# Optimization experiments

Hardware: AMD Instinct MI355X
Metric: run time of the kernel (lower is better)

The kernel has to match this reference:

```python
import jax, jax.numpy as jnp
import numpy as np

B, T, I, H, G = 4096, 1024, 1, 16, 48  # G = 3*H gates

def _gru_layer(inp, w_ih, w_hh, b_ih, b_hh):
    # inp: [B, T, Din] -> out: [B, T, H]. PyTorch GRU gate math.
    # Precompute all input-side gate projections once (batched GEMM).
    xg = jnp.einsum('btd,gd->tbg', inp, w_ih) + b_ih  # [T, B, 3H]

    def step(h, xg_t):
        hg = h @ w_hh.T + b_hh                         # [B, 3H]
        xr, xz, xn = jnp.split(xg_t, 3, axis=-1)
        hr, hz, hn = jnp.split(hg, 3, axis=-1)
        r = jax.nn.sigmoid(xr + hr)
        z = jax.nn.sigmoid(xz + hz)
        n = jnp.tanh(xn + r * hn)
        h_new = (1.0 - z) * n + z * h
        return h_new, h_new

    h0 = jnp.zeros((inp.shape[0], H), dtype=inp.dtype)
    _, ys = jax.lax.scan(step, h0, xg)                 # ys: [T, B, H]
    return jnp.transpose(ys, (1, 0, 2))                # [B, T, H]

def setup_inputs() -> dict:
    key = jax.random.key(0)
    ks = jax.random.split(key, 8)
    s = 1.0 / np.sqrt(H)  # PyTorch default uniform(-1/sqrt(H), 1/sqrt(H))
    u = lambda k, shape: jax.random.uniform(k, shape, jnp.float32, -s, s)
    return {
        'x':      jax.random.normal(ks[0], (B, T, I), jnp.float32),
        'w_ih0':  u(ks[1], (G, I)),
        'w_ih12': u(ks[2], (2, G, H)),
        'w_hh':   u(ks[3], (3, G, H)),
        'b_ih':   u(ks[4], (3, G)),
        'b_hh':   u(ks[5], (3, G)),
        'fc_w':   u(ks[6], (5, H)),
        'fc_b':   u(ks[7], (5,)),
    }

def reference(x, w_ih0, w_ih12, w_hh, b_ih, b_hh, fc_w, fc_b):
    # 3-layer GRU (dropout=0.3 between layers is identity in eval mode)
    h = _gru_layer(x, w_ih0,     w_hh[0], b_ih[0], b_hh[0])
    h = _gru_layer(h, w_ih12[0], w_hh[1], b_ih[1], b_hh[1])
    h = _gru_layer(h, w_ih12[1], w_hh[2], b_ih[2], b_hh[2])
    # Linear head on the last timestep
    return h[:, -1, :] @ fc_w.T + fc_b                 # [B, 5]
```

## Files before the change

kernel.cpp:

```cpp
#include <hip/hip_runtime.h>
#include <stdint.h>

#define TSTEPS 1024
#define S 4
#define NK 258
#define L2E 1.4426950408889634f
#define XPITCH 1028

typedef float v2f __attribute__((ext_vector_type(2)));
typedef float v4f __attribute__((ext_vector_type(4)));

__device__ __forceinline__ float rcpf_(float v) { return __builtin_amdgcn_rcpf(v); }
__device__ __forceinline__ float ex2(float v) { return __builtin_amdgcn_exp2f(v); }
#define PKFMA(a, b, c) __builtin_elementwise_fma((a), (b), (c))

__device__ __forceinline__ v2f ldg2(const float* p) {
    v2f r; uint64_t a = (uint64_t)p;
    asm volatile("global_load_dwordx2 %0, %1, off\n\ts_waitcnt vmcnt(0)"
                 : "=v"(r) : "v"(a));
    return r;
}
__device__ __forceinline__ float ldg1(const float* p) {
    float r; uint64_t a = (uint64_t)p;
    asm volatile("global_load_dword %0, %1, off\n\ts_waitcnt vmcnt(0)"
                 : "=v"(r) : "v"(a));
    return r;
}

#define RDH(dst, p)                                                        \
    do {                                                                   \
        v4f a0 = *(const v4f*)(p);                                         \
        v4f a1 = *(const v4f*)((p) + 4);                                   \
        v4f a2 = *(const v4f*)((p) + 8);                                   \
        v4f a3 = *(const v4f*)((p) + 12);                                  \
        dst[0] = __builtin_shufflevector(a0, a0, 0, 1);                    \
        dst[1] = __builtin_shufflevector(a0, a0, 2, 3);                    \
        dst[2] = __builtin_shufflevector(a1, a1, 0, 1);                    \
        dst[3] = __builtin_shufflevector(a1, a1, 2, 3);                    \
        dst[4] = __builtin_shufflevector(a2, a2, 0, 1);                    \
        dst[5] = __builtin_shufflevector(a2, a2, 2, 3);                    \
        dst[6] = __builtin_shufflevector(a3, a3, 0, 1);                    \
        dst[7] = __builtin_shufflevector(a3, a3, 2, 3);                    \
    } while (0)

#define DOT8(w, h, seed)                                                   \
    ({                                                                     \
        v2f _a = PKFMA(w[0], h[0], (seed));                                \
        _a = PKFMA(w[1], h[1], _a); _a = PKFMA(w[2], h[2], _a);            \
        _a = PKFMA(w[3], h[3], _a); _a = PKFMA(w[4], h[4], _a);            \
        _a = PKFMA(w[5], h[5], _a); _a = PKFMA(w[6], h[6], _a);            \
        _a = PKFMA(w[7], h[7], _a);                                        \
        _a.x + _a.y;                                                       \
    })
#define DOT16(wa, ha, wb, hb, seed)                                        \
    ({                                                                     \
        v2f _a = PKFMA(wa[0], ha[0], (seed));                              \
        _a = PKFMA(wa[1], ha[1], _a); _a = PKFMA(wa[2], ha[2], _a);        \
        _a = PKFMA(wa[3], ha[3], _a); _a = PKFMA(wa[4], ha[4], _a);        \
        _a = PKFMA(wa[5], ha[5], _a); _a = PKFMA(wa[6], ha[6], _a);        \
        _a = PKFMA(wa[7], ha[7], _a);                                      \
        _a = PKFMA(wb[0], hb[0], _a); _a = PKFMA(wb[1], hb[1], _a);        \
        _a = PKFMA(wb[2], hb[2], _a); _a = PKFMA(wb[3], hb[3], _a);        \
        _a = PKFMA(wb[4], hb[4], _a); _a = PKFMA(wb[5], hb[5], _a);        \
        _a = PKFMA(wb[6], hb[6], _a); _a = PKFMA(wb[7], hb[7], _a);        \
        _a.x + _a.y;                                                       \
    })

__global__ __launch_bounds__(192, 3)
__attribute__((amdgpu_waves_per_eu(3, 3)))
void gru3_sk(
    const float* __restrict__ x,
    const float* __restrict__ w_ih0,
    const float* __restrict__ w_ih12,
    const float* __restrict__ w_hh,
    const float* __restrict__ b_ih,
    const float* __restrict__ b_hh,
    const float* __restrict__ fc_w,
    const float* __restrict__ fc_b,
    float* __restrict__ out)
{
    __shared__ float xs[4][XPITCH];
    __shared__ float hring[3][2][S][4][16];
    __shared__ float h2f[4][16];

    const int tid = threadIdx.x;
    const int role = tid >> 6;
    const int lane = tid & 63;
    const int s = lane >> 4;
    const int u = lane & 15;
    const int seq = blockIdx.x * 4 + s;

    {
        const float4* xg = (const float4*)(x + (size_t)blockIdx.x * 4 * TSTEPS);
#pragma unroll
        for (int j = 0; j < 6; ++j) {
            int idx = tid + 192 * j;
            if (idx < 1024) {
                float4 v = xg[idx];
                *(float4*)&xs[idx >> 8][(idx & 255) * 4] = v;
            }
        }
#pragma unroll
        for (int j = 0; j < 8; ++j)
            ((float*)hring)[tid + 192 * j] = 0.f;
    }
    __syncthreads();

    if (role == 0) {
        v2f wr[8], wz[8], wn[8];
#pragma unroll
        for (int m = 0; m < 8; ++m) {
            wr[m] = ldg2(w_hh + (u) * 16 + 2 * m) * -L2E;
            wz[m] = ldg2(w_hh + (16 + u) * 16 + 2 * m) * -L2E;
            wn[m] = ldg2(w_hh + (32 + u) * 16 + 2 * m) * (2.f * L2E);
        }
        const float wxr = ldg1(w_ih0 + u) * -L2E;
        const float wxz = ldg1(w_ih0 + 16 + u) * -L2E;
        const float wxn = ldg1(w_ih0 + 32 + u) * (2.f * L2E);
        const v2f sbr = {-(ldg1(b_ih + u) + ldg1(b_hh + u)) * L2E, 0.f};
        const v2f sbz = {-(ldg1(b_ih + 16 + u) + ldg1(b_hh + 16 + u)) * L2E, 0.f};
        const v2f sbn = {ldg1(b_hh + 32 + u) * (2.f * L2E), 0.f};
        const float bnx = ldg1(b_ih + 32 + u) * (2.f * L2E);
        float* cur = &hring[0][0][0][s][0];
        float* prv = &hring[0][1][0][s][0];
        float hown = 0.f;
        for (int K = 0; K < NK; ++K) {
            if (K < 256) {
                v4f xq = *(const v4f*)&xs[s][K * S];
#pragma unroll
                for (int j = 0; j < S; ++j) {
                    const float* rb = (j == 0) ? (prv + (S - 1) * 64)
                                               : (cur + (j - 1) * 64);
                    v2f hp[8];
                    RDH(hp, rb);
                    float xt = xq[j];
                    float sr = fmaf(wxr, xt, DOT8(wr, hp, sbr));
                    float sz = fmaf(wxz, xt, DOT8(wz, hp, sbz));
                    float snh = DOT8(wn, hp, sbn);
                    float r = rcpf_(1.f + ex2(sr));
                    float z = rcpf_(1.f + ex2(sz));
                    float ut = fmaf(r, snh, fmaf(wxn, xt, bnx));
                    float n = fmaf(-2.f, rcpf_(ex2(ut) + 1.f), 1.f);
                    hown = fmaf(z, hown - n, n);
                    cur[j * 64 + u] = hown;
                }
            }
            __syncthreads();
            float* t_ = cur; cur = prv; prv = t_;
        }
    } else if (role == 1) {
        v2f wr[8], wz[8], wn[8], vr[8], vz[8], vn[8];
#pragma unroll
        for (int m = 0; m < 8; ++m) {
            wr[m] = ldg2(w_hh + (48 + u) * 16 + 2 * m) * -L2E;
            wz[m] = ldg2(w_hh + (48 + 16 + u) * 16 + 2 * m) * -L2E;
            wn[m] = ldg2(w_hh + (48 + 32 + u) * 16 + 2 * m) * (2.f * L2E);
            vr[m] = ldg2(w_ih12 + (u) * 16 + 2 * m) * -L2E;
            vz[m] = ldg2(w_ih12 + (16 + u) * 16 + 2 * m) * -L2E;
            vn[m] = ldg2(w_ih12 + (32 + u) * 16 + 2 * m) * (2.f * L2E);
        }
        const v2f sbr = {-(ldg1(b_ih + 48 + u) + ldg1(b_hh + 48 + u)) * L2E, 0.f};
        const v2f sbz = {-(ldg1(b_ih + 64 + u) + ldg1(b_hh + 64 + u)) * L2E, 0.f};
        const v2f sbn = {ldg1(b_hh + 80 + u) * (2.f * L2E), 0.f};
        const v2f sbx = {ldg1(b_ih + 80 + u) * (2.f * L2E), 0.f};
        float* in0 = &hring[0][0][0][s][0];
        float* in1 = &hring[0][1][0][s][0];
        float* my0 = &hring[1][0][0][s][0];
        float* my1 = &hring[1][1][0][s][0];
        float* inp = in1;
        float* mycur = my0; float* myprv = my1;
        float hown = 0.f;
        for (int K = 0; K < NK; ++K) {
            if (K >= 1 && K < 257) {
#pragma unroll
                for (int j = 0; j < S; ++j) {
                    const float* rin = inp + j * 64;
                    const float* rown = (j == 0) ? (myprv + (S - 1) * 64)
                                                 : (mycur + (j - 1) * 64);
                    v2f hin[8], hp[8];
                    RDH(hin, rin);
                    RDH(hp, rown);
                    float sr = DOT16(wr, hp, vr, hin, sbr);
                    float sz = DOT16(wz, hp, vz, hin, sbz);
                    float snh = DOT8(wn, hp, sbn);
                    float snx = DOT8(vn, hin, sbx);
                    float r = rcpf_(1.f + ex2(sr));
                    float z = rcpf_(1.f + ex2(sz));
                    float ut = fmaf(r, snh, snx);
                    float n = fmaf(-2.f, rcpf_(ex2(ut) + 1.f), 1.f);
                    hown = fmaf(z, hown - n, n);
                    mycur[j * 64 + u] = hown;
                }
            }
            __syncthreads();
            float* t_ = inp == in0 ? in1 : in0; inp = t_;
            t_ = mycur; mycur = myprv; myprv = t_;
        }
    } else {
        v2f wr[8], wz[8], wn[8], vr[8], vz[8], vn[8];
#pragma unroll
        for (int m = 0; m < 8; ++m) {
            wr[m] = ldg2(w_hh + (96 + u) * 16 + 2 * m) * -L2E;
            wz[m] = ldg2(w_hh + (96 + 16 + u) * 16 + 2 * m) * -L2E;
            wn[m] = ldg2(w_hh + (96 + 32 + u) * 16 + 2 * m) * (2.f * L2E);
            vr[m] = ldg2(w_ih12 + (48 + u) * 16 + 2 * m) * -L2E;
            vz[m] = ldg2(w_ih12 + (48 + 16 + u) * 16 + 2 * m) * -L2E;
            vn[m] = ldg2(w_ih12 + (48 + 32 + u) * 16 + 2 * m) * (2.f * L2E);
        }
        const v2f sbr = {-(ldg1(b_ih + 96 + u) + ldg1(b_hh + 96 + u)) * L2E, 0.f};
        const v2f sbz = {-(ldg1(b_ih + 112 + u) + ldg1(b_hh + 112 + u)) * L2E, 0.f};
        const v2f sbn = {ldg1(b_hh + 128 + u) * (2.f * L2E), 0.f};
        const v2f sbx = {ldg1(b_ih + 128 + u) * (2.f * L2E), 0.f};
        float* in0 = &hring[1][0][0][s][0];
        float* in1 = &hring[1][1][0][s][0];
        float* my0 = &hring[2][0][0][s][0];
        float* my1 = &hring[2][1][0][s][0];
        float* inp = in1;
        float* mycur = my0; float* myprv = my1;
        float hown = 0.f;
        for (int K = 0; K < NK; ++K) {
            if (K >= 2) {
#pragma unroll
                for (int j = 0; j < S; ++j) {
                    const float* rin = inp + j * 64;
                    const float* rown = (j == 0) ? (myprv + (S - 1) * 64)
                                                 : (mycur + (j - 1) * 64);
                    v2f hin[8], hp[8];
                    RDH(hin, rin);
                    RDH(hp, rown);
                    float sr = DOT16(wr, hp, vr, hin, sbr);
                    float sz = DOT16(wz, hp, vz, hin, sbz);
                    float snh = DOT8(wn, hp, sbn);
                    float snx = DOT8(vn, hin, sbx);
                    float r = rcpf_(1.f + ex2(sr));
                    float z = rcpf_(1.f + ex2(sz));
                    float ut = fmaf(r, snh, snx);
                    float n = fmaf(-2.f, rcpf_(ex2(ut) + 1.f), 1.f);
                    hown = fmaf(z, hown - n, n);
                    mycur[j * 64 + u] = hown;
                }
            }
            __syncthreads();
            float* t_ = inp == in0 ? in1 : in0; inp = t_;
            t_ = mycur; mycur = myprv; myprv = t_;
        }
        h2f[s][u] = hown;
        if (u < 5) {
            float acc = fc_b[u];
#pragma unroll
            for (int j = 0; j < 16; ++j)
                acc = fmaf(fc_w[u * 16 + j], h2f[s][j], acc);
            out[seq * 5 + u] = acc;
        }
    }
}

extern "C" void kernel_launch(void* const* d_in, const int* in_sizes, int n_in,
                              void* d_out, int out_size, void* d_ws, size_t ws_size,
                              hipStream_t stream) {
    const float* x      = (const float*)d_in[0];
    const float* w_ih0  = (const float*)d_in[1];
    const float* w_ih12 = (const float*)d_in[2];
    const float* w_hh   = (const float*)d_in[3];
    const float* b_ih   = (const float*)d_in[4];
    const float* b_hh   = (const float*)d_in[5];
    const float* fc_w   = (const float*)d_in[6];
    const float* fc_b   = (const float*)d_in[7];
    float* out = (float*)d_out;

    gru3_sk<<<1024, 192, 0, stream>>>(
        x, w_ih0, w_ih12, w_hh, b_ih, b_hh, fc_w, fc_b, out);
}
```

Measured before the change: 492.3 us.

## Have each layer compute the next layer's input projections and drop the x LDS staging

Each producer wave now computes the next layer's input-side gate projections (W_ih·h plus bias) right after updating its hidden state and writes them to a shared ring. The consumer layer only reads three scalars per step instead of a 16-wide vector, which shortens its recurrence-critical dot products from 32-length to 16-length. The hidden state is kept in a tiny per-layer scratch in LDS, and x is streamed directly from global memory with a one-step prefetch instead of being staged in LDS. This balances work across the three pipeline waves and cuts LDS use, but it relies on wave-level ordering of the LDS write and the immediate read-back of h within a single wave, and it adds global-load latency for x.

```diff
diff --git a/kernel.cpp b/kernel.cpp
--- a/kernel.cpp
+++ b/kernel.cpp
@@ -5,7 +5,6 @@
 #define S 4
 #define NK 258
 #define L2E 1.4426950408889634f
-#define XPITCH 1028
 
 typedef float v2f __attribute__((ext_vector_type(2)));
 typedef float v4f __attribute__((ext_vector_type(4)));
@@ -52,23 +51,10 @@
         _a = PKFMA(w[7], h[7], _a);                                        \
         _a.x + _a.y;                                                       \
     })
-#define DOT16(wa, ha, wb, hb, seed)                                        \
-    ({                                                                     \
-        v2f _a = PKFMA(wa[0], ha[0], (seed));                              \
-        _a = PKFMA(wa[1], ha[1], _a); _a = PKFMA(wa[2], ha[2], _a);        \
-        _a = PKFMA(wa[3], ha[3], _a); _a = PKFMA(wa[4], ha[4], _a);        \
-        _a = PKFMA(wa[5], ha[5], _a); _a = PKFMA(wa[6], ha[6], _a);        \
-        _a = PKFMA(wa[7], ha[7], _a);                                      \
-        _a = PKFMA(wb[0], hb[0], _a); _a = PKFMA(wb[1], hb[1], _a);        \
-        _a = PKFMA(wb[2], hb[2], _a); _a = PKFMA(wb[3], hb[3], _a);        \
-        _a = PKFMA(wb[4], hb[4], _a); _a = PKFMA(wb[5], hb[5], _a);        \
-        _a = PKFMA(wb[6], hb[6], _a); _a = PKFMA(wb[7], hb[7], _a);        \
-        _a.x + _a.y;                                                       \
-    })
 
 __global__ __launch_bounds__(192, 3)
 __attribute__((amdgpu_waves_per_eu(3, 3)))
-void gru3_sk(
+void gru3_po(
     const float* __restrict__ x,
     const float* __restrict__ w_ih0,
     const float* __restrict__ w_ih12,
@@ -79,9 +65,8 @@
     const float* __restrict__ fc_b,
     float* __restrict__ out)
 {
-    __shared__ float xs[4][XPITCH];
-    __shared__ float hring[3][2][S][4][16];
-    __shared__ float h2f[4][16];
+    __shared__ float pring[2][2][S][4][48];
+    __shared__ float hscr[3][4][16];
 
     const int tid = threadIdx.x;
     const int role = tid >> 6;
@@ -90,29 +75,19 @@
     const int u = lane & 15;
     const int seq = blockIdx.x * 4 + s;
 
-    {
-        const float4* xg = (const float4*)(x + (size_t)blockIdx.x * 4 * TSTEPS);
-#pragma unroll
-        for (int j = 0; j < 6; ++j) {
-            int idx = tid + 192 * j;
-            if (idx < 1024) {
-                float4 v = xg[idx];
-                *(float4*)&xs[idx >> 8][(idx & 255) * 4] = v;
-            }
-        }
-#pragma unroll
-        for (int j = 0; j < 8; ++j)
-            ((float*)hring)[tid + 192 * j] = 0.f;
-    }
+    ((float*)hscr)[tid] = 0.f;
     __syncthreads();
 
     if (role == 0) {
-        v2f wr[8], wz[8], wn[8];
+        v2f wr[8], wz[8], wn[8], v1r[8], v1z[8], v1n[8];
 #pragma unroll
         for (int m = 0; m < 8; ++m) {
             wr[m] = ldg2(w_hh + (u) * 16 + 2 * m) * -L2E;
             wz[m] = ldg2(w_hh + (16 + u) * 16 + 2 * m) * -L2E;
             wn[m] = ldg2(w_hh + (32 + u) * 16 + 2 * m) * (2.f * L2E);
+            v1r[m] = ldg2(w_ih12 + (u) * 16 + 2 * m) * -L2E;
+            v1z[m] = ldg2(w_ih12 + (16 + u) * 16 + 2 * m) * -L2E;
+            v1n[m] = ldg2(w_ih12 + (32 + u) * 16 + 2 * m) * (2.f * L2E);
         }
         const float wxr = ldg1(w_ih0 + u) * -L2E;
         const float wxz = ldg1(w_ih0 + 16 + u) * -L2E;
@@ -121,18 +96,23 @@
         const v2f sbz = {-(ldg1(b_ih + 16 + u) + ldg1(b_hh + 16 + u)) * L2E, 0.f};
         const v2f sbn = {ldg1(b_hh + 32 + u) * (2.f * L2E), 0.f};
         const float bnx = ldg1(b_ih + 32 + u) * (2.f * L2E);
-        float* cur = &hring[0][0][0][s][0];
-        float* prv = &hring[0][1][0][s][0];
+        const v2f s1r = {-(ldg1(b_ih + 48 + u) + ldg1(b_hh + 48 + u)) * L2E, 0.f};
+        const v2f s1z = {-(ldg1(b_ih + 64 + u) + ldg1(b_hh + 64 + u)) * L2E, 0.f};
+        const v2f s1x = {ldg1(b_ih + 80 + u) * (2.f * L2E), 0.f};
+
+        const float* xp = x + (size_t)seq * TSTEPS;
+        const float* hr = &hscr[0][s][0];
+        float* pc = &pring[0][0][0][s][0];
+        float* pp = &pring[0][1][0][s][0];
         float hown = 0.f;
+        v4f xq = *(const v4f*)xp;
         for (int K = 0; K < NK; ++K) {
             if (K < 256) {
-                v4f xq = *(const v4f*)&xs[s][K * S];
+                v4f xqn = *(const v4f*)(xp + 4 * ((K < 255) ? K + 1 : 255));
 #pragma unroll
                 for (int j = 0; j < S; ++j) {
-                    const float* rb = (j == 0) ? (prv + (S - 1) * 64)
-                                               : (cur + (j - 1) * 64);
                     v2f hp[8];
-                    RDH(hp, rb);
+                    RDH(hp, hr);
                     float xt = xq[j];
                     float sr = fmaf(wxr, xt, DOT8(wr, hp, sbr));
                     float sz = fmaf(wxz, xt, DOT8(wz, hp, sbz));
@@ -142,116 +122,119 @@
                     float ut = fmaf(r, snh, fmaf(wxn, xt, bnx));
                     float n = fmaf(-2.f, rcpf_(ex2(ut) + 1.f), 1.f);
                     hown = fmaf(z, hown - n, n);
-                    cur[j * 64 + u] = hown;
+                    hscr[0][s][u] = hown;
+                    v2f hq[8];
+                    RDH(hq, hr);
+                    float pr = DOT8(v1r, hq, s1r);
+                    float pz = DOT8(v1z, hq, s1z);
+                    float px = DOT8(v1n, hq, s1x);
+                    float* pb = pc + j * (4 * 48);
+                    pb[u] = pr; pb[16 + u] = pz; pb[32 + u] = px;
                 }
+                xq = xqn;
             }
             __syncthreads();
-            float* t_ = cur; cur = prv; prv = t_;
+            float* t_ = pc; pc = pp; pp = t_;
         }
     } else if (role == 1) {
-        v2f wr[8], wz[8], wn[8], vr[8], vz[8], vn[8];
+        v2f wr[8], wz[8], wn[8], v2r[8], v2z[8], v2n[8];
 #pragma unroll
         for (int m = 0; m < 8; ++m) {
             wr[m] = ldg2(w_hh + (48 + u) * 16 + 2 * m) * -L2E;
             wz[m] = ldg2(w_hh + (48 + 16 + u) * 16 + 2 * m) * -L2E;
             wn[m] = ldg2(w_hh + (48 + 32 + u) * 16 + 2 * m) * (2.f * L2E);
-            vr[m] = ldg2(w_ih12 + (u) * 16 + 2 * m) * -L2E;
-            vz[m] = ldg2(w_ih12 + (16 + u) * 16 + 2 * m) * -L2E;
-            vn[m] = ldg2(w_ih12 + (32 + u) * 16 + 2 * m) * (2.f * L2E);
-        }
-        const v2f sbr = {-(ldg1(b_ih + 48 + u) + ldg1(b_hh + 48 + u)) * L2E, 0.f};
-        const v2f sbz = {-(ldg1(b_ih + 64 + u) + ldg1(b_hh + 64 + u)) * L2E, 0.f};
+            v2r[m] = ldg2(w_ih12 + (48 + u) * 16 + 2 * m) * -L2E;
+            v2z[m] = ldg2(w_ih12 + (48 + 16 + u) * 16 + 2 * m) * -L2E;
+            v2n[m] = ldg2(w_ih12 + (48 + 32 + u) * 16 + 2 * m) * (2.f * L2E);
+        }
         const v2f sbn = {ldg1(b_hh + 80 + u) * (2.f * L2E), 0.f};
-        const v2f sbx = {ldg1(b_ih + 80 + u) * (2.f * L2E), 0.f};
-        float* in0 = &hring[0][0][0][s][0];
-        float* in1 = &hring[0][1][0][s][0];
-        float* my0 = &hring[1][0][0][s][0];
-        float* my1 = &hring[1][1][0][s][0];
-        float* inp = in1;
+        const v2f s2r = {-(ldg1(b_ih + 96 + u) + ldg1(b_hh + 96 + u)) * L2E, 0.f};
+        const v2f s2z = {-(ldg1(b_ih + 112 + u) + ldg1(b_hh + 112 + u)) * L2E, 0.f};
+        const v2f s2x = {ldg1(b_ih + 128 + u) * (2.f * L2E), 0.f};
+
+        const float* hr = &hscr[1][s][0];
+        const float* in0 = &pring[0][0][0][s][0];
+        const float* in1 = &pring[0][1][0][s][0];
+        float* my0 = &pring[1][0][0][s][0];
+        float* my1 = &pring[1][1][0][s][0];
+        const float* inp = in1;
         float* mycur = my0; float* myprv = my1;
         float hown = 0.f;
         for (int K = 0; K < NK; ++K) {
             if (K >= 1 && K < 257) {
 #pragma unroll
                 for (int j = 0; j < S; ++j) {
-                    const float* rin = inp + j * 64;
-                    const float* rown = (j == 0) ? (myprv + (S - 1) * 64)
-                                                 : (mycur + (j - 1) * 64);
-                    v2f hin[8], hp[8];
-                    RDH(hin, rin);
-                    RDH(hp, rown);
-                    float sr = DOT16(wr, hp, vr, hin, sbr);
-                    float sz = DOT16(wz, hp, vz, hin, sbz);
+                    const float* qb = inp + j * (4 * 48);
+                    float pr = qb[u], pz = qb[16 + u], px = qb[32 + u];
+                    v2f hp[8];
+                    RDH(hp, hr);
+                    float sr = DOT8(wr, hp, ((v2f){pr, 0.f}));
+                    float sz = DOT8(wz, hp, ((v2f){pz, 0.f}));
                     float snh = DOT8(wn, hp, sbn);
-                    float snx = DOT8(vn, hin, sbx);
                     float r = rcpf_(1.f + ex2(sr));
                     float z = rcpf_(1.f + ex2(sz));
-                    float ut = fmaf(r, snh, snx);
+                    float ut = fmaf(r, snh, px);
                     float n = fmaf(-2.f, rcpf_(ex2(ut) + 1.f), 1.f);
                     hown = fmaf(z, hown - n, n);
-                    mycur[j * 64 + u] = hown;
+                    hscr[1][s][u] = hown;
+                    v2f hq[8];
+                    RDH(hq, hr);
+                    float qr = DOT8(v2r, hq, s2r);
+                    float qz = DOT8(v2z, hq, s2z);
+                    float qx = DOT8(v2n, hq, s2x);
+                    float* pb = mycur + j * (4 * 48);
+                    pb[u] = qr; pb[16 + u] = qz; pb[32 + u] = qx;
                 }
             }
             __syncthreads();
-            float* t_ = inp == in0 ? in1 : in0; inp = t_;
-            t_ = mycur; mycur = myprv; myprv = t_;
+            const float* t0 = (inp == in0) ? in1 : in0; inp = t0;
+            float* t1 = mycur; mycur = myprv; myprv = t1;
         }
     } else {
-        v2f wr[8], wz[8], wn[8], vr[8], vz[8], vn[8];
+        v2f wr[8], wz[8], wn[8];
 #pragma unroll
         for (int m = 0; m < 8; ++m) {
             wr[m] = ldg2(w_hh + (96 + u) * 16 + 2 * m) * -L2E;
             wz[m] = ldg2(w_hh + (96 + 16 + u) * 16 + 2 * m) * -L2E;
             wn[m] = ldg2(w_hh + (96 + 32 + u) * 16 + 2 * m) * (2.f * L2E);
-            vr[m] = ldg2(w_ih12 + (48 + u) * 16 + 2 * m) * -L2E;
-            vz[m] = ldg2(w_ih12 + (48 + 16 + u) * 16 + 2 * m) * -L2E;
-            vn[m] = ldg2(w_ih12 + (48 + 32 + u) * 16 + 2 * m) * (2.f * L2E);
-        }
-        const v2f sbr = {-(ldg1(b_ih + 96 + u) + ldg1(b_hh + 96 + u)) * L2E, 0.f};
-        const v2f sbz = {-(ldg1(b_ih + 112 + u) + ldg1(b_hh + 112 + u)) * L2E, 0.f};
+        }
         const v2f sbn = {ldg1(b_hh + 128 + u) * (2.f * L2E), 0.f};
-        const v2f sbx = {ldg1(b_ih + 128 + u) * (2.f * L2E), 0.f};
-        float* in0 = &hring[1][0][0][s][0];
-        float* in1 = &hring[1][1][0][s][0];
-        float* my0 = &hring[2][0][0][s][0];
-        float* my1 = &hring[2][1][0][s][0];
-        float* inp = in1;
-        float* mycur = my0; float* myprv = my1;
+
+        const float* hr = &hscr[2][s][0];
+        const float* in0 = &pring[1][0][0][s][0];
+        const float* in1 = &pring[1][1][0][s][0];
+        const float* inp = in1;
         float hown = 0.f;
         for (int K = 0; K < NK; ++K) {
             if (K >= 2) {
 #pragma unroll
                 for (int j = 0; j < S; ++j) {
-                    const float* rin = inp + j * 64;
-                    const float* rown = (j == 0) ? (myprv + (S - 1) * 64)
-                                                 : (mycur + (j - 1) * 64);
-                    v2f hin[8], hp[8];
-                    RDH(hin, rin);
-                    RDH(hp, rown);
-                    float sr = DOT16(wr, hp, vr, hin, sbr);
-                    float sz = DOT16(wz, hp, vz, hin, sbz);
+                    const float* qb = inp + j * (4 * 48);
+                    float pr = qb[u], pz = qb[16 + u], px = qb[32 + u];
+                    v2f hp[8];
+                    RDH(hp, hr);
+                    float sr = DOT8(wr, hp, ((v2f){pr, 0.f}));
+                    float sz = DOT8(wz, hp, ((v2f){pz, 0.f}));
                     float snh = DOT8(wn, hp, sbn);
-                    float snx = DOT8(vn, hin, sbx);
                     float r = rcpf_(1.f + ex2(sr));
                     float z = rcpf_(1.f + ex2(sz));
-                    float ut = fmaf(r, snh, snx);
+                    float ut = fmaf(r, snh, px);
                     float n = fmaf(-2.f, rcpf_(ex2(ut) + 1.f), 1.f);
                     hown = fmaf(z, hown - n, n);
-                    mycur[j * 64 + u] = hown;
+                    hscr[2][s][u] = hown;
                 }
             }
             __syncthreads();
-            float* t_ = inp == in0 ? in1 : in0; inp = t_;
-            t_ = mycur; mycur = myprv; myprv = t_;
-        }
-        h2f[s][u] = hown;
-        if (u < 5) {
-            float acc = fc_b[u];
-#pragma unroll
-            for (int j = 0; j < 16; ++j)
-                acc = fmaf(fc_w[u * 16 + j], h2f[s][j], acc);
-            out[seq * 5 + u] = acc;
-        }
+            const float* t0 = (inp == in0) ? in1 : in0; inp = t0;
+        }
+        v2f hf[8];
+        RDH(hf, hr);
+        const int ur = (u < 5) ? u : 0;
+        v2f fw[8];
+#pragma unroll
+        for (int m = 0; m < 8; ++m) fw[m] = ldg2(fc_w + ur * 16 + 2 * m);
+        float acc = ldg1(fc_b + ur) + DOT8(fw, hf, ((v2f){0.f, 0.f}));
+        if (u < 5) out[seq * 5 + u] = acc;
     }
 }
 
@@ -268,6 +251,6 @@
     const float* fc_b   = (const float*)d_in[7];
     float* out = (float*)d_out;
 
-    gru3_sk<<<1024, 192, 0, stream>>>(
+    gru3_po<<<1024, 192, 0, stream>>>(
         x, w_ih0, w_ih12, w_hh, b_ih, b_hh, fc_w, fc_b, out);
 }
```

Result: slower. 511.8 us (+4.0%).
